# Optimization experiments

Measured on AMD Instinct MI355X. Metric: run time of the kernel, lower is better.

Reference implementation:

```python
import jax, jax.numpy as jnp
import numpy as np

N = 100000
E = 1600000
IN_FEATS = 128
N_HIDDEN = 128
N_CLASSES = 40
KLIST = [2, 2, 2]  # k=6 split over 3 layers as in DeepSGC.__init__


def setup_inputs() -> dict:
    key = jax.random.key(0)
    ks = jax.random.split(key, 10)
    features = jax.random.normal(ks[0], (N, IN_FEATS), dtype=jnp.float32)
    src = jax.random.randint(ks[1], (E,), 0, N, dtype=jnp.int64 if jax.config.jax_enable_x64 else jnp.int32)
    dst = jax.random.randint(ks[2], (E,), 0, N, dtype=jnp.int64 if jax.config.jax_enable_x64 else jnp.int32)
    def glorot(k, fan_in, fan_out):
        lim = (6.0 / (fan_in + fan_out)) ** 0.5
        return jax.random.uniform(k, (fan_in, fan_out), jnp.float32, -lim, lim)
    W1 = glorot(ks[3], IN_FEATS, N_HIDDEN)
    b1 = jnp.zeros((N_HIDDEN,), jnp.float32)
    W2 = glorot(ks[4], N_HIDDEN, N_HIDDEN)
    b2 = jnp.zeros((N_HIDDEN,), jnp.float32)
    W3 = glorot(ks[5], N_HIDDEN, N_CLASSES)
    b3 = jnp.zeros((N_CLASSES,), jnp.float32)
    return {"features": features, "src": src, "dst": dst,
            "W1": W1, "b1": b1, "W2": W2, "b2": b2, "W3": W3, "b3": b3}


def _propagate(h, src, dst, norm, k):
    # k hops of symmetric-normalized adjacency SpMM: h <- D^{-1/2} A D^{-1/2} h
    for _ in range(k):
        h = h * norm  # pre-scale [N, d]
        h = jax.ops.segment_sum(h[src], dst, num_segments=N)  # scatter-add over edges
        h = h * norm  # post-scale
    return h


def reference(features, src, dst, W1, b1, W2, b2, W3, b3):
    # in-degree based symmetric norm, clamped to >= 1 (as DGL SGConv)
    deg = jax.ops.segment_sum(jnp.ones((E,), jnp.float32), dst, num_segments=N)
    norm = jax.lax.rsqrt(jnp.clip(deg, 1.0))[:, None]  # [N, 1]

    h = features
    # layer 1: SGConv(k=2) + relu (dropout p=0 -> identity)
    h = _propagate(h, src, dst, norm, KLIST[0]) @ W1 + b1
    h = jax.nn.relu(h)
    # layer 2
    h = _propagate(h, src, dst, norm, KLIST[1]) @ W2 + b2
    h = jax.nn.relu(h)
    # layer 3 (no activation)
    h = _propagate(h, src, dst, norm, KLIST[2]) @ W3 + b3
    return h
```

## Files before the change

kernel.cpp:

```cpp
#include <hip/hip_runtime.h>
#include <hip/hip_bf16.h>


typedef __attribute__((ext_vector_type(8))) short short8v;
typedef __attribute__((ext_vector_type(4))) float f32x4;
typedef __attribute__((ext_vector_type(2))) unsigned int u32x2;

#define SBLK 128

__device__ __forceinline__ unsigned short f2bf(float x) {
    unsigned int u = __builtin_bit_cast(unsigned int, x);
    unsigned int r = u + 0x7fffu + ((u >> 16) & 1u);
    return (unsigned short)(r >> 16);
}
__device__ __forceinline__ float bf2f(unsigned short h) {
    unsigned int u = ((unsigned int)h) << 16;
    return __builtin_bit_cast(float, u);
}


__global__ void __launch_bounds__(256) deg_rank_kernel(const int* __restrict__ dst,
                                                       int* __restrict__ deg,
                                                       int* __restrict__ rank, int E) {
    int e = blockIdx.x * blockDim.x + threadIdx.x;
    if (e < E) rank[e] = atomicAdd(&deg[dst[e]], 1);
}

__global__ void __launch_bounds__(256) scanA_kernel(const int* __restrict__ deg,
                                                    int* __restrict__ rowptr,
                                                    int* __restrict__ bsum,
                                                    float* __restrict__ norm,
                                                    int n, int seg) {
    __shared__ int ws[4];
    __shared__ int carry;
    int b = blockIdx.x;
    int start = b * seg;
    int finish = start + seg; if (finish > n) finish = n;
    int t = threadIdx.x, lane = t & 63, w = t >> 6;
    if (t == 0) carry = 0;
    __syncthreads();
    for (int base = start; base < finish; base += 256) {
        int i = base + t;
        int v = 0;
        if (i < finish) {
            v = deg[i];
            norm[i] = rsqrtf((float)(v < 1 ? 1 : v));
        }
        int x = v;
        #pragma unroll
        for (int off = 1; off < 64; off <<= 1) {
            int y = __shfl_up(x, off, 64);
            if (lane >= off) x += y;
        }
        if (lane == 63) ws[w] = x;
        __syncthreads();
        int woff = 0;
        #pragma unroll
        for (int k = 0; k < 4; ++k) if (k < w) woff += ws[k];
        if (i < finish) rowptr[i] = carry + woff + x - v;
        int tot = ws[0] + ws[1] + ws[2] + ws[3];
        __syncthreads();
        if (t == 0) carry += tot;
        __syncthreads();
    }
    if (t == 0) bsum[b] = carry;
}

__global__ void __launch_bounds__(256) scanC_kernel(int* __restrict__ rowptr,
                                                    const int* __restrict__ bsum,
                                                    int n, int seg) {
    __shared__ int tmp[SBLK + 1];
    int b = blockIdx.x, t = threadIdx.x;
    if (t < SBLK) tmp[t] = bsum[t];
    __syncthreads();
    if (t == 0) {
        int s = 0;
        #pragma unroll 4
        for (int i = 0; i < SBLK; ++i) { int v = tmp[i]; tmp[i] = s; s += v; }
        tmp[SBLK] = s;
    }
    __syncthreads();
    int add = tmp[b];
    int start = b * seg;
    int finish = start + seg; if (finish > n) finish = n;
    for (int i = start + t; i < finish; i += 256) rowptr[i] += add;
    if (b == 0 && t == 0) rowptr[n] = tmp[SBLK];
}

__global__ void __launch_bounds__(256) fill_kernel(const int* __restrict__ src,
                                                   const int* __restrict__ dst,
                                                   const int* __restrict__ rowptr,
                                                   const int* __restrict__ rank,
                                                   int* __restrict__ col, int E) {
    int e = blockIdx.x * blockDim.x + threadIdx.x;
    if (e < E) col[rowptr[dst[e]] + rank[e]] = src[e];
}


__global__ void __launch_bounds__(256) xquant_kernel(const float4* __restrict__ x,
                                                     const float* __restrict__ norm,
                                                     u32x2* __restrict__ xq,
                                                     float* __restrict__ S,
                                                     float* __restrict__ Sn,
                                                     int n) {
    int gw = (blockIdx.x * blockDim.x + threadIdx.x) >> 6;
    int lane = threadIdx.x & 63, half = lane >> 5, l32 = lane & 31;
    int node = gw * 2 + half;
    if (node >= n) return;
    float4 v = x[(size_t)node * 32 + l32];
    float m = fmaxf(fmaxf(fabsf(v.x), fabsf(v.y)), fmaxf(fabsf(v.z), fabsf(v.w)));
    #pragma unroll
    for (int s = 1; s < 32; s <<= 1) m = fmaxf(m, __shfl_xor(m, s));
    float sraw = fmaxf(m, 1e-30f);
    float inv = 32767.f / sraw;
    float sv = sraw * (1.f / 32767.f);
    int a0 = (int)rintf(fminf(fmaxf(v.x * inv, -32767.f), 32767.f));
    int a1 = (int)rintf(fminf(fmaxf(v.y * inv, -32767.f), 32767.f));
    int a2 = (int)rintf(fminf(fmaxf(v.z * inv, -32767.f), 32767.f));
    int a3 = (int)rintf(fminf(fmaxf(v.w * inv, -32767.f), 32767.f));
    u32x2 p = {(unsigned)(a0 & 0xffff) | ((unsigned)a1 << 16),
               (unsigned)(a2 & 0xffff) | ((unsigned)a3 << 16)};
    __builtin_nontemporal_store(p, &xq[(size_t)node * 32 + l32]);
    if (l32 == 0) { S[node] = sv; Sn[node] = sv * norm[node]; }
}


template <int EPI>
__global__ void __launch_bounds__(256) spmm128_q(const u32x2* __restrict__ hq,
                                                 const float* __restrict__ esc,
                                                 const int* __restrict__ rp,
                                                 const int* __restrict__ col,
                                                 const float* __restrict__ norm,
                                                 u32x2* __restrict__ outq,
                                                 float* __restrict__ So,
                                                 float* __restrict__ Sno,
                                                 u32x2* __restrict__ Hi,
                                                 u32x2* __restrict__ Lo,
                                                 int n) {
    int wid = (blockIdx.x * blockDim.x + threadIdx.x) >> 6;
    if (wid >= n) return;
    int lane = threadIdx.x & 63, half = lane >> 5, l32 = lane & 31;
    int beg = rp[wid], end = rp[wid + 1];
    f32x4 acc = {0.f, 0.f, 0.f, 0.f};
    if (beg < end) {
        int last = end - 1;
        for (int e = beg; e < end; e += 8) {
            int i0 = e + half, i1 = e + 2 + half, i2 = e + 4 + half, i3 = e + 6 + half;
            int i0c = i0 < end ? i0 : last;
            int i1c = i1 < end ? i1 : last;
            int i2c = i2 < end ? i2 : last;
            int i3c = i3 < end ? i3 : last;
            int u0 = col[i0c], u1 = col[i1c], u2 = col[i2c], u3 = col[i3c];
            float s0 = i0 < end ? esc[u0] : 0.f;
            float s1 = i1 < end ? esc[u1] : 0.f;
            float s2 = i2 < end ? esc[u2] : 0.f;
            float s3 = i3 < end ? esc[u3] : 0.f;
            u32x2 q0 = hq[(size_t)u0 * 32 + l32];
            u32x2 q1 = hq[(size_t)u1 * 32 + l32];
            u32x2 q2 = hq[(size_t)u2 * 32 + l32];
            u32x2 q3 = hq[(size_t)u3 * 32 + l32];
            acc.x += (float)(short)(q0.x) * s0;
            acc.y += (float)((int)q0.x >> 16) * s0;
            acc.z += (float)(short)(q0.y) * s0;
            acc.w += (float)((int)q0.y >> 16) * s0;
            acc.x += (float)(short)(q1.x) * s1;
            acc.y += (float)((int)q1.x >> 16) * s1;
            acc.z += (float)(short)(q1.y) * s1;
            acc.w += (float)((int)q1.y >> 16) * s1;
            acc.x += (float)(short)(q2.x) * s2;
            acc.y += (float)((int)q2.x >> 16) * s2;
            acc.z += (float)(short)(q2.y) * s2;
            acc.w += (float)((int)q2.y >> 16) * s2;
            acc.x += (float)(short)(q3.x) * s3;
            acc.y += (float)((int)q3.x >> 16) * s3;
            acc.z += (float)(short)(q3.y) * s3;
            acc.w += (float)((int)q3.y >> 16) * s3;
        }
    }
    acc.x += __shfl_xor(acc.x, 32);
    acc.y += __shfl_xor(acc.y, 32);
    acc.z += __shfl_xor(acc.z, 32);
    acc.w += __shfl_xor(acc.w, 32);
    float nv = norm[wid];
    if (EPI == 0) {
        float f = nv * nv;
        acc.x *= f; acc.y *= f; acc.z *= f; acc.w *= f;
        float m = fmaxf(fmaxf(fabsf(acc.x), fabsf(acc.y)), fmaxf(fabsf(acc.z), fabsf(acc.w)));
        #pragma unroll
        for (int s = 1; s < 64; s <<= 1) m = fmaxf(m, __shfl_xor(m, s));
        float sraw = fmaxf(m, 1e-30f);
        float inv = 32767.f / sraw;
        float sv = sraw * (1.f / 32767.f);
        if (half == 0) {
            int a0 = (int)rintf(fminf(fmaxf(acc.x * inv, -32767.f), 32767.f));
            int a1 = (int)rintf(fminf(fmaxf(acc.y * inv, -32767.f), 32767.f));
            int a2 = (int)rintf(fminf(fmaxf(acc.z * inv, -32767.f), 32767.f));
            int a3 = (int)rintf(fminf(fmaxf(acc.w * inv, -32767.f), 32767.f));
            u32x2 p = {(unsigned)(a0 & 0xffff) | ((unsigned)a1 << 16),
                       (unsigned)(a2 & 0xffff) | ((unsigned)a3 << 16)};
            __builtin_nontemporal_store(p, &outq[(size_t)wid * 32 + l32]);
        }
        if (lane == 0) { So[wid] = sv; Sno[wid] = sv * nv; }
    } else {
        if (half == 0) {
            float v0 = acc.x * nv, v1 = acc.y * nv, v2 = acc.z * nv, v3 = acc.w * nv;
            unsigned short h0 = f2bf(v0), h1 = f2bf(v1), h2 = f2bf(v2), h3 = f2bf(v3);
            unsigned short l0 = f2bf(v0 - bf2f(h0)), l1 = f2bf(v1 - bf2f(h1));
            unsigned short l2 = f2bf(v2 - bf2f(h2)), l3 = f2bf(v3 - bf2f(h3));
            u32x2 hp = {(unsigned int)h0 | ((unsigned int)h1 << 16),
                        (unsigned int)h2 | ((unsigned int)h3 << 16)};
            u32x2 lp = {(unsigned int)l0 | ((unsigned int)l1 << 16),
                        (unsigned int)l2 | ((unsigned int)l3 << 16)};
            __builtin_nontemporal_store(hp, &Hi[(size_t)wid * 32 + l32]);
            __builtin_nontemporal_store(lp, &Lo[(size_t)wid * 32 + l32]);
        }
    }
}

template <int FIRST, int BIAS>
__global__ void __launch_bounds__(256) spmm40_kernel(const f32x4* __restrict__ hin,
                                                     f32x4* __restrict__ hout,
                                                     const int* __restrict__ rp,
                                                     const int* __restrict__ col,
                                                     const float* __restrict__ norm,
                                                     const float* __restrict__ b3,
                                                     int n) {
    int wid = (blockIdx.x * blockDim.x + threadIdx.x) >> 6;
    if (wid >= n) return;
    int lane = threadIdx.x & 63;
    int slot = lane / 10;
    int t = lane % 10;
    bool active = slot < 6;
    int beg = rp[wid], end = rp[wid + 1];
    f32x4 acc = {0.f, 0.f, 0.f, 0.f};
    if (beg < end) {
        int last = end - 1;
        for (int base = beg; base < end; base += 18) {
            int i0 = base + slot, i1 = base + 6 + slot, i2 = base + 12 + slot;
            int i0c = (active && i0 < end) ? i0 : last;
            int i1c = (active && i1 < end) ? i1 : last;
            int i2c = (active && i2 < end) ? i2 : last;
            int u0 = col[i0c], u1 = col[i1c], u2 = col[i2c];
            float s0 = (active && i0 < end) ? (FIRST ? norm[u0] : 1.f) : 0.f;
            float s1 = (active && i1 < end) ? (FIRST ? norm[u1] : 1.f) : 0.f;
            float s2 = (active && i2 < end) ? (FIRST ? norm[u2] : 1.f) : 0.f;
            f32x4 x0 = hin[(size_t)u0 * 10 + t];
            f32x4 x1 = hin[(size_t)u1 * 10 + t];
            f32x4 x2 = hin[(size_t)u2 * 10 + t];
            acc.x += x0.x * s0; acc.y += x0.y * s0; acc.z += x0.z * s0; acc.w += x0.w * s0;
            acc.x += x1.x * s1; acc.y += x1.y * s1; acc.z += x1.z * s1; acc.w += x1.w * s1;
            acc.x += x2.x * s2; acc.y += x2.y * s2; acc.z += x2.z * s2; acc.w += x2.w * s2;
        }
    }
    f32x4 tot = acc;
    #pragma unroll
    for (int k = 1; k < 6; ++k) {
        int srcl = (lane % 10) + ((slot + k) % 6) * 10;
        tot.x += __shfl(acc.x, srcl);
        tot.y += __shfl(acc.y, srcl);
        tot.z += __shfl(acc.z, srcl);
        tot.w += __shfl(acc.w, srcl);
    }
    if (slot == 0) {
        float nv = norm[wid];
        float f = FIRST ? nv * nv : nv;
        f32x4 o = {tot.x * f, tot.y * f, tot.z * f, tot.w * f};
        if (BIAS) {
            f32x4 bv = ((const f32x4*)b3)[t];
            o.x += bv.x; o.y += bv.y; o.z += bv.z; o.w += bv.w;
        }
        __builtin_nontemporal_store(o, &hout[(size_t)wid * 10 + t]);
    }
}


__device__ __forceinline__ void wprep_one(const float* __restrict__ W,
                                          short* __restrict__ Wh,
                                          short* __restrict__ Wl,
                                          int ncols, int CF, int i) {
    int j = i & 7;
    int lane = (i >> 3) & 63;
    int f = i >> 9;
    int cf = f % CF, ks = f / CF;
    int k = ks * 32 + 8 * (lane >> 4) + j;
    int c = cf * 16 + (lane & 15);
    float v = (c < ncols) ? W[k * ncols + c] : 0.f;
    unsigned short h = f2bf(v);
    unsigned short l = f2bf(v - bf2f(h));
    Wh[i] = (short)h;
    Wl[i] = (short)l;
}

__global__ void __launch_bounds__(256) wprep_all(const float* __restrict__ W1,
                                                 const float* __restrict__ W2,
                                                 const float* __restrict__ W3,
                                                 short* __restrict__ W1h, short* __restrict__ W1l,
                                                 short* __restrict__ W2h, short* __restrict__ W2l,
                                                 short* __restrict__ W3h, short* __restrict__ W3l) {
    int i = blockIdx.x * blockDim.x + threadIdx.x;
    if (i < 16384) wprep_one(W1, W1h, W1l, 128, 8, i);
    else if (i < 32768) wprep_one(W2, W2h, W2l, 128, 8, i - 16384);
    else if (i < 38912) wprep_one(W3, W3h, W3l, 40, 3, i - 32768);
}


template <int MODE>
__global__ void __launch_bounds__(256) gemm_mfma128(const unsigned short* __restrict__ Ahi,
                                                    const unsigned short* __restrict__ Alo,
                                                    const short8v* __restrict__ Wh,
                                                    const short8v* __restrict__ Wl,
                                                    const float* __restrict__ bias,
                                                    const float* __restrict__ norm,
                                                    unsigned short* __restrict__ Cq,
                                                    float* __restrict__ So,
                                                    float* __restrict__ Sno,
                                                    unsigned short* __restrict__ Chi,
                                                    unsigned short* __restrict__ Clo,
                                                    int n) {
    int lane = threadIdx.x & 63;
    int wid = threadIdx.x >> 6;
    int r0 = blockIdx.x * 64 + wid * 16;
    if (r0 >= n) return;
    int arow = r0 + (lane & 15);
    if (arow > n - 1) arow = n - 1;
    int kbase = 8 * (lane >> 4);
    f32x4 acc[8];
    #pragma unroll
    for (int i = 0; i < 8; ++i) acc[i] = (f32x4){0.f, 0.f, 0.f, 0.f};
    #pragma unroll
    for (int ks = 0; ks < 4; ++ks) {
        short8v ah = *(const short8v*)(Ahi + (size_t)arow * 128 + ks * 32 + kbase);
        short8v al = *(const short8v*)(Alo + (size_t)arow * 128 + ks * 32 + kbase);
        #pragma unroll
        for (int cf = 0; cf < 8; ++cf) {
            short8v bh = Wh[(ks * 8 + cf) * 64 + lane];
            short8v bl = Wl[(ks * 8 + cf) * 64 + lane];
            acc[cf] = __builtin_amdgcn_mfma_f32_16x16x32_bf16(ah, bh, acc[cf], 0, 0, 0);
            acc[cf] = __builtin_amdgcn_mfma_f32_16x16x32_bf16(al, bh, acc[cf], 0, 0, 0);
            acc[cf] = __builtin_amdgcn_mfma_f32_16x16x32_bf16(ah, bl, acc[cf], 0, 0, 0);
        }
    }
    int rbase = r0 + (lane >> 4) * 4;
    int c0 = lane & 15;
    float bc[8];
    #pragma unroll
    for (int cf = 0; cf < 8; ++cf) bc[cf] = bias[cf * 16 + c0];

    if (MODE == 0) {
        float mq[4] = {0.f, 0.f, 0.f, 0.f};
        #pragma unroll
        for (int cf = 0; cf < 8; ++cf) {
            #pragma unroll
            for (int q = 0; q < 4; ++q)
                mq[q] = fmaxf(mq[q], fmaxf(acc[cf][q] + bc[cf], 0.f));
        }
        #pragma unroll
        for (int s = 1; s < 16; s <<= 1) {
            #pragma unroll
            for (int q = 0; q < 4; ++q) mq[q] = fmaxf(mq[q], __shfl_xor(mq[q], s));
        }
        float invq[4], svq[4];
        #pragma unroll
        for (int q = 0; q < 4; ++q) {
            float sraw = fmaxf(mq[q], 1e-30f);
            invq[q] = 32767.f / sraw;
            svq[q] = sraw * (1.f / 32767.f);
        }
        #pragma unroll
        for (int cf = 0; cf < 8; ++cf) {
            int colc = cf * 16 + c0;
            #pragma unroll
            for (int q = 0; q < 4; ++q) {
                int row = rbase + q;
                if (row >= n) continue;
                float v = fmaxf(acc[cf][q] + bc[cf], 0.f);
                int qi = (int)rintf(fminf(v * invq[q], 32767.f));
                Cq[(size_t)row * 128 + colc] = (unsigned short)qi;
            }
        }
        if (c0 == 0) {
            #pragma unroll
            for (int q = 0; q < 4; ++q) {
                int row = rbase + q;
                if (row < n) { So[row] = svq[q]; Sno[row] = svq[q] * norm[row]; }
            }
        }
    } else {
        #pragma unroll
        for (int cf = 0; cf < 8; ++cf) {
            int colc = cf * 16 + c0;
            #pragma unroll
            for (int q = 0; q < 4; ++q) {
                int row = rbase + q;
                if (row >= n) continue;
                float v = fmaxf(acc[cf][q] + bc[cf], 0.f);
                unsigned short h = f2bf(v);
                unsigned short l = f2bf(v - bf2f(h));
                Chi[(size_t)row * 128 + colc] = h;
                Clo[(size_t)row * 128 + colc] = l;
            }
        }
    }
}

__global__ void __launch_bounds__(256) gemm_mfma40(const unsigned short* __restrict__ Ahi,
                                                   const unsigned short* __restrict__ Alo,
                                                   const short8v* __restrict__ Wh,
                                                   const short8v* __restrict__ Wl,
                                                   float* __restrict__ Cf, int n) {
    int lane = threadIdx.x & 63;
    int wid = threadIdx.x >> 6;
    int r0 = blockIdx.x * 64 + wid * 16;
    if (r0 >= n) return;
    int arow = r0 + (lane & 15);
    if (arow > n - 1) arow = n - 1;
    int kbase = 8 * (lane >> 4);
    f32x4 acc[3];
    #pragma unroll
    for (int i = 0; i < 3; ++i) acc[i] = (f32x4){0.f, 0.f, 0.f, 0.f};
    #pragma unroll
    for (int ks = 0; ks < 4; ++ks) {
        short8v ah = *(const short8v*)(Ahi + (size_t)arow * 128 + ks * 32 + kbase);
        short8v al = *(const short8v*)(Alo + (size_t)arow * 128 + ks * 32 + kbase);
        #pragma unroll
        for (int cf = 0; cf < 3; ++cf) {
            short8v bh = Wh[(ks * 3 + cf) * 64 + lane];
            short8v bl = Wl[(ks * 3 + cf) * 64 + lane];
            acc[cf] = __builtin_amdgcn_mfma_f32_16x16x32_bf16(ah, bh, acc[cf], 0, 0, 0);
            acc[cf] = __builtin_amdgcn_mfma_f32_16x16x32_bf16(al, bh, acc[cf], 0, 0, 0);
            acc[cf] = __builtin_amdgcn_mfma_f32_16x16x32_bf16(ah, bl, acc[cf], 0, 0, 0);
        }
    }
    int rbase = r0 + (lane >> 4) * 4;
    int c0 = lane & 15;
    #pragma unroll
    for (int cf = 0; cf < 3; ++cf) {
        int colc = cf * 16 + c0;
        if (colc >= 40) continue;
        #pragma unroll
        for (int q = 0; q < 4; ++q) {
            int row = rbase + q;
            if (row >= n) continue;
            Cf[(size_t)row * 40 + colc] = acc[cf][q];
        }
    }
}


extern "C" void kernel_launch(void* const* d_in, const int* in_sizes, int n_in,
                              void* d_out, int out_size, void* d_ws, size_t ws_size,
                              hipStream_t stream) {
    const float* features = (const float*)d_in[0];
    const int*   src      = (const int*)d_in[1];
    const int*   dst      = (const int*)d_in[2];
    const float* W1 = (const float*)d_in[3];
    const float* b1 = (const float*)d_in[4];
    const float* W2 = (const float*)d_in[5];
    const float* b2 = (const float*)d_in[6];
    const float* W3 = (const float*)d_in[7];
    const float* b3 = (const float*)d_in[8];
    float* out = (float*)d_out;

    const int N = in_sizes[0] / 128;
    const int E = in_sizes[1];

    char* ws = (char*)d_ws;
    size_t off = 0;
    auto alloc = [&](size_t bytes) -> void* {
        void* p = ws + off;
        off += (bytes + 511) & ~(size_t)511;
        return p;
    };
    u32x2* Xq  = (u32x2*)alloc((size_t)N * 32 * sizeof(u32x2));
    u32x2* F1q = (u32x2*)alloc((size_t)N * 32 * sizeof(u32x2));
    u32x2* F2q = (u32x2*)alloc((size_t)N * 32 * sizeof(u32x2));
    unsigned short* Hi = (unsigned short*)alloc((size_t)N * 128 * sizeof(unsigned short));
    unsigned short* Lo = (unsigned short*)alloc((size_t)N * 128 * sizeof(unsigned short));
    float* Sx  = (float*)alloc((size_t)N * sizeof(float));
    float* Snx = (float*)alloc((size_t)N * sizeof(float));
    float* S1  = (float*)alloc((size_t)N * sizeof(float));
    float* Sn1 = (float*)alloc((size_t)N * sizeof(float));
    float* S2  = (float*)alloc((size_t)N * sizeof(float));
    float* Sn2 = (float*)alloc((size_t)N * sizeof(float));
    int*   col    = (int*)alloc((size_t)E * sizeof(int));
    int*   deg    = (int*)alloc((size_t)N * sizeof(int));
    int*   rowptr = (int*)alloc((size_t)(N + 1) * sizeof(int));
    float* norm   = (float*)alloc((size_t)N * sizeof(float));
    int*   bsum   = (int*)alloc((size_t)(SBLK + 2) * sizeof(int));
    short* W1h = (short*)alloc(16384 * sizeof(short));
    short* W1l = (short*)alloc(16384 * sizeof(short));
    short* W2h = (short*)alloc(16384 * sizeof(short));
    short* W2l = (short*)alloc(16384 * sizeof(short));
    short* W3h = (short*)alloc(6144 * sizeof(short));
    short* W3l = (short*)alloc(6144 * sizeof(short));
    int*   rank = (int*)Hi;
    float* G40a = (float*)F2q;
    float* G40b = (float*)Xq;

    const int seg = (N + SBLK - 1) / SBLK;
    const int eblocks = (E + 255) / 256;

    hipMemsetAsync(deg, 0, (size_t)N * sizeof(int), stream);
    deg_rank_kernel<<<eblocks, 256, 0, stream>>>(dst, deg, rank, E);
    scanA_kernel<<<SBLK, 256, 0, stream>>>(deg, rowptr, bsum, norm, N, seg);
    scanC_kernel<<<SBLK, 256, 0, stream>>>(rowptr, bsum, N, seg);
    fill_kernel<<<eblocks, 256, 0, stream>>>(src, dst, rowptr, rank, col, E);

    wprep_all<<<(38912 + 255) / 256, 256, 0, stream>>>(W1, W2, W3, W1h, W1l, W2h, W2l, W3h, W3l);
    {
        int waves2 = (N + 1) / 2;
        int xblocks = (waves2 * 64 + 255) / 256;
        xquant_kernel<<<xblocks, 256, 0, stream>>>((const float4*)features, norm, Xq, Sx, Snx, N);
    }

    const int spmm_blocks = (N * 64 + 255) / 256;
    const int gemm_blocks = (N + 63) / 64;

    spmm128_q<0><<<spmm_blocks, 256, 0, stream>>>(Xq, Snx, rowptr, col, norm,
                                                  F1q, S1, Sn1, nullptr, nullptr, N);
    spmm128_q<1><<<spmm_blocks, 256, 0, stream>>>(F1q, S1, rowptr, col, norm,
                                                  nullptr, nullptr, nullptr, (u32x2*)Hi, (u32x2*)Lo, N);
    gemm_mfma128<0><<<gemm_blocks, 256, 0, stream>>>(Hi, Lo, (const short8v*)W1h, (const short8v*)W1l,
                                                     b1, norm, (unsigned short*)F2q, S2, Sn2,
                                                     nullptr, nullptr, N);

    spmm128_q<0><<<spmm_blocks, 256, 0, stream>>>(F2q, Sn2, rowptr, col, norm,
                                                  F1q, S1, Sn1, nullptr, nullptr, N);
    spmm128_q<1><<<spmm_blocks, 256, 0, stream>>>(F1q, S1, rowptr, col, norm,
                                                  nullptr, nullptr, nullptr, (u32x2*)Hi, (u32x2*)Lo, N);
    gemm_mfma128<1><<<gemm_blocks, 256, 0, stream>>>(Hi, Lo, (const short8v*)W2h, (const short8v*)W2l,
                                                     b2, norm, nullptr, nullptr, nullptr,
                                                     Hi, Lo, N);

    gemm_mfma40<<<gemm_blocks, 256, 0, stream>>>(Hi, Lo, (const short8v*)W3h, (const short8v*)W3l, G40a, N);
    spmm40_kernel<1, 0><<<spmm_blocks, 256, 0, stream>>>((const f32x4*)G40a, (f32x4*)G40b, rowptr, col, norm, nullptr, N);
    spmm40_kernel<0, 1><<<spmm_blocks, 256, 0, stream>>>((const f32x4*)G40b, (f32x4*)out, rowptr, col, norm, b3, N);
}
```

Baseline: 639.6 us.

## Quantize layer-3 path to int16 with per-row scales and deepen SpMM gather unroll

Layer 2's GEMM now writes int16-quantized rows with per-row scales instead of bf16 hi/lo pairs. The 40-wide GEMM dequantizes these on the fly, and the two final 40-column SpMMs gather int16 rows instead of fp32. This halves the bytes moved in the last layer's gathers and GEMM input. The 128-wide SpMM gather loop is also unrolled from 4 to 8 edges per half-wave to keep more loads in flight. The cost is extra quantization error in the last layer and higher register pressure in the SpMM.

After: 690.6 us. 1.08x slower.

```diff
diff --git a/kernel.cpp b/kernel.cpp
--- a/kernel.cpp
+++ b/kernel.cpp
@@ -100,7 +100,6 @@
 __global__ void __launch_bounds__(256) xquant_kernel(const float4* __restrict__ x,
                                                      const float* __restrict__ norm,
                                                      u32x2* __restrict__ xq,
-                                                     float* __restrict__ S,
                                                      float* __restrict__ Sn,
                                                      int n) {
     int gw = (blockIdx.x * blockDim.x + threadIdx.x) >> 6;
@@ -121,7 +120,7 @@
     u32x2 p = {(unsigned)(a0 & 0xffff) | ((unsigned)a1 << 16),
                (unsigned)(a2 & 0xffff) | ((unsigned)a3 << 16)};
     __builtin_nontemporal_store(p, &xq[(size_t)node * 32 + l32]);
-    if (l32 == 0) { S[node] = sv; Sn[node] = sv * norm[node]; }
+    if (l32 == 0) Sn[node] = sv * norm[node];
 }
 
 
@@ -133,7 +132,6 @@
                                                  const float* __restrict__ norm,
                                                  u32x2* __restrict__ outq,
                                                  float* __restrict__ So,
-                                                 float* __restrict__ Sno,
                                                  u32x2* __restrict__ Hi,
                                                  u32x2* __restrict__ Lo,
                                                  int n) {
@@ -144,37 +142,24 @@
     f32x4 acc = {0.f, 0.f, 0.f, 0.f};
     if (beg < end) {
         int last = end - 1;
-        for (int e = beg; e < end; e += 8) {
-            int i0 = e + half, i1 = e + 2 + half, i2 = e + 4 + half, i3 = e + 6 + half;
-            int i0c = i0 < end ? i0 : last;
-            int i1c = i1 < end ? i1 : last;
-            int i2c = i2 < end ? i2 : last;
-            int i3c = i3 < end ? i3 : last;
-            int u0 = col[i0c], u1 = col[i1c], u2 = col[i2c], u3 = col[i3c];
-            float s0 = i0 < end ? esc[u0] : 0.f;
-            float s1 = i1 < end ? esc[u1] : 0.f;
-            float s2 = i2 < end ? esc[u2] : 0.f;
-            float s3 = i3 < end ? esc[u3] : 0.f;
-            u32x2 q0 = hq[(size_t)u0 * 32 + l32];
-            u32x2 q1 = hq[(size_t)u1 * 32 + l32];
-            u32x2 q2 = hq[(size_t)u2 * 32 + l32];
-            u32x2 q3 = hq[(size_t)u3 * 32 + l32];
-            acc.x += (float)(short)(q0.x) * s0;
-            acc.y += (float)((int)q0.x >> 16) * s0;
-            acc.z += (float)(short)(q0.y) * s0;
-            acc.w += (float)((int)q0.y >> 16) * s0;
-            acc.x += (float)(short)(q1.x) * s1;
-            acc.y += (float)((int)q1.x >> 16) * s1;
-            acc.z += (float)(short)(q1.y) * s1;
-            acc.w += (float)((int)q1.y >> 16) * s1;
-            acc.x += (float)(short)(q2.x) * s2;
-            acc.y += (float)((int)q2.x >> 16) * s2;
-            acc.z += (float)(short)(q2.y) * s2;
-            acc.w += (float)((int)q2.y >> 16) * s2;
-            acc.x += (float)(short)(q3.x) * s3;
-            acc.y += (float)((int)q3.x >> 16) * s3;
-            acc.z += (float)(short)(q3.y) * s3;
-            acc.w += (float)((int)q3.y >> 16) * s3;
+        for (int e = beg; e < end; e += 16) {
+            float s[8];
+            u32x2 q[8];
+            #pragma unroll
+            for (int k = 0; k < 8; ++k) {
+                int i = e + 2 * k + half;
+                int ic = i < end ? i : last;
+                int u = col[ic];
+                s[k] = i < end ? esc[u] : 0.f;
+                q[k] = hq[(size_t)u * 32 + l32];
+            }
+            #pragma unroll
+            for (int k = 0; k < 8; ++k) {
+                acc.x += (float)(short)(q[k].x) * s[k];
+                acc.y += (float)((int)q[k].x >> 16) * s[k];
+                acc.z += (float)(short)(q[k].y) * s[k];
+                acc.w += (float)((int)q[k].y >> 16) * s[k];
+            }
         }
     }
     acc.x += __shfl_xor(acc.x, 32);
@@ -200,7 +185,7 @@
                        (unsigned)(a2 & 0xffff) | ((unsigned)a3 << 16)};
             __builtin_nontemporal_store(p, &outq[(size_t)wid * 32 + l32]);
         }
-        if (lane == 0) { So[wid] = sv; Sno[wid] = sv * nv; }
+        if (lane == 0) So[wid] = sv;
     } else {
         if (half == 0) {
             float v0 = acc.x * nv, v1 = acc.y * nv, v2 = acc.z * nv, v3 = acc.w * nv;
@@ -217,14 +202,18 @@
     }
 }
 
-template <int FIRST, int BIAS>
-__global__ void __launch_bounds__(256) spmm40_kernel(const f32x4* __restrict__ hin,
-                                                     f32x4* __restrict__ hout,
-                                                     const int* __restrict__ rp,
-                                                     const int* __restrict__ col,
-                                                     const float* __restrict__ norm,
-                                                     const float* __restrict__ b3,
-                                                     int n) {
+
+template <int EPI>
+__global__ void __launch_bounds__(256) spmm40_q(const u32x2* __restrict__ hq,
+                                                const float* __restrict__ esc,
+                                                const int* __restrict__ rp,
+                                                const int* __restrict__ col,
+                                                const float* __restrict__ norm,
+                                                u32x2* __restrict__ outq,
+                                                float* __restrict__ So,
+                                                f32x4* __restrict__ outf,
+                                                const float* __restrict__ b3,
+                                                int n) {
     int wid = (blockIdx.x * blockDim.x + threadIdx.x) >> 6;
     if (wid >= n) return;
     int lane = threadIdx.x & 63;
@@ -236,40 +225,63 @@
     if (beg < end) {
         int last = end - 1;
         for (int base = beg; base < end; base += 18) {
-            int i0 = base + slot, i1 = base + 6 + slot, i2 = base + 12 + slot;
-            int i0c = (active && i0 < end) ? i0 : last;
-            int i1c = (active && i1 < end) ? i1 : last;
-            int i2c = (active && i2 < end) ? i2 : last;
-            int u0 = col[i0c], u1 = col[i1c], u2 = col[i2c];
-            float s0 = (active && i0 < end) ? (FIRST ? norm[u0] : 1.f) : 0.f;
-            float s1 = (active && i1 < end) ? (FIRST ? norm[u1] : 1.f) : 0.f;
-            float s2 = (active && i2 < end) ? (FIRST ? norm[u2] : 1.f) : 0.f;
-            f32x4 x0 = hin[(size_t)u0 * 10 + t];
-            f32x4 x1 = hin[(size_t)u1 * 10 + t];
-            f32x4 x2 = hin[(size_t)u2 * 10 + t];
-            acc.x += x0.x * s0; acc.y += x0.y * s0; acc.z += x0.z * s0; acc.w += x0.w * s0;
-            acc.x += x1.x * s1; acc.y += x1.y * s1; acc.z += x1.z * s1; acc.w += x1.w * s1;
-            acc.x += x2.x * s2; acc.y += x2.y * s2; acc.z += x2.z * s2; acc.w += x2.w * s2;
+            float s[3];
+            u32x2 q[3];
+            #pragma unroll
+            for (int k = 0; k < 3; ++k) {
+                int i = base + 6 * k + slot;
+                int ic = (active && i < end) ? i : last;
+                int u = col[ic];
+                s[k] = (active && i < end) ? esc[u] : 0.f;
+                q[k] = hq[(size_t)u * 10 + t];
+            }
+            #pragma unroll
+            for (int k = 0; k < 3; ++k) {
+                acc.x += (float)(short)(q[k].x) * s[k];
+                acc.y += (float)((int)q[k].x >> 16) * s[k];
+                acc.z += (float)(short)(q[k].y) * s[k];
+                acc.w += (float)((int)q[k].y >> 16) * s[k];
+            }
         }
     }
     f32x4 tot = acc;
     #pragma unroll
     for (int k = 1; k < 6; ++k) {
-        int srcl = (lane % 10) + ((slot + k) % 6) * 10;
+        int srcl = t + ((slot + k) % 6) * 10;
         tot.x += __shfl(acc.x, srcl);
         tot.y += __shfl(acc.y, srcl);
         tot.z += __shfl(acc.z, srcl);
         tot.w += __shfl(acc.w, srcl);
     }
-    if (slot == 0) {
-        float nv = norm[wid];
-        float f = FIRST ? nv * nv : nv;
-        f32x4 o = {tot.x * f, tot.y * f, tot.z * f, tot.w * f};
-        if (BIAS) {
+    float nv = norm[wid];
+    if (EPI == 0) {
+        float f = nv * nv;
+        f32x4 v = {tot.x * f, tot.y * f, tot.z * f, tot.w * f};
+        float m = (slot < 6)
+                ? fmaxf(fmaxf(fabsf(v.x), fabsf(v.y)), fmaxf(fabsf(v.z), fabsf(v.w)))
+                : 0.f;
+        #pragma unroll
+        for (int s = 1; s < 64; s <<= 1) m = fmaxf(m, __shfl_xor(m, s));
+        float sraw = fmaxf(m, 1e-30f);
+        float inv = 32767.f / sraw;
+        float sv = sraw * (1.f / 32767.f);
+        if (slot == 0) {
+            int a0 = (int)rintf(fminf(fmaxf(v.x * inv, -32767.f), 32767.f));
+            int a1 = (int)rintf(fminf(fmaxf(v.y * inv, -32767.f), 32767.f));
+            int a2 = (int)rintf(fminf(fmaxf(v.z * inv, -32767.f), 32767.f));
+            int a3 = (int)rintf(fminf(fmaxf(v.w * inv, -32767.f), 32767.f));
+            u32x2 p = {(unsigned)(a0 & 0xffff) | ((unsigned)a1 << 16),
+                       (unsigned)(a2 & 0xffff) | ((unsigned)a3 << 16)};
+            __builtin_nontemporal_store(p, &outq[(size_t)wid * 10 + t]);
+        }
+        if (lane == 0) So[wid] = sv;
+    } else {
+        if (slot == 0) {
             f32x4 bv = ((const f32x4*)b3)[t];
-            o.x += bv.x; o.y += bv.y; o.z += bv.z; o.w += bv.w;
-        }
-        __builtin_nontemporal_store(o, &hout[(size_t)wid * 10 + t]);
+            f32x4 o = {tot.x * nv + bv.x, tot.y * nv + bv.y,
+                       tot.z * nv + bv.z, tot.w * nv + bv.w};
+            __builtin_nontemporal_store(o, &outf[(size_t)wid * 10 + t]);
+        }
     }
 }
 
@@ -304,7 +316,6 @@
 }
 
 
-template <int MODE>
 __global__ void __launch_bounds__(256) gemm_mfma128(const unsigned short* __restrict__ Ahi,
                                                     const unsigned short* __restrict__ Alo,
                                                     const short8v* __restrict__ Wh,
@@ -314,8 +325,6 @@
                                                     unsigned short* __restrict__ Cq,
                                                     float* __restrict__ So,
                                                     float* __restrict__ Sno,
-                                                    unsigned short* __restrict__ Chi,
-                                                    unsigned short* __restrict__ Clo,
                                                     int n) {
     int lane = threadIdx.x & 63;
     int wid = threadIdx.x >> 6;
@@ -346,68 +355,55 @@
     #pragma unroll
     for (int cf = 0; cf < 8; ++cf) bc[cf] = bias[cf * 16 + c0];
 
-    if (MODE == 0) {
-        float mq[4] = {0.f, 0.f, 0.f, 0.f};
-        #pragma unroll
-        for (int cf = 0; cf < 8; ++cf) {
-            #pragma unroll
-            for (int q = 0; q < 4; ++q)
-                mq[q] = fmaxf(mq[q], fmaxf(acc[cf][q] + bc[cf], 0.f));
-        }
-        #pragma unroll
-        for (int s = 1; s < 16; s <<= 1) {
-            #pragma unroll
-            for (int q = 0; q < 4; ++q) mq[q] = fmaxf(mq[q], __shfl_xor(mq[q], s));
-        }
-        float invq[4], svq[4];
+    float mq[4] = {0.f, 0.f, 0.f, 0.f};
+    #pragma unroll
+    for (int cf = 0; cf < 8; ++cf) {
+        #pragma unroll
+        for (int q = 0; q < 4; ++q)
+            mq[q] = fmaxf(mq[q], fmaxf(acc[cf][q] + bc[cf], 0.f));
+    }
+    #pragma unroll
+    for (int s = 1; s < 16; s <<= 1) {
+        #pragma unroll
+        for (int q = 0; q < 4; ++q) mq[q] = fmaxf(mq[q], __shfl_xor(mq[q], s));
+    }
+    float invq[4], svq[4];
+    #pragma unroll
+    for (int q = 0; q < 4; ++q) {
+        float sraw = fmaxf(mq[q], 1e-30f);
+        invq[q] = 32767.f / sraw;
+        svq[q] = sraw * (1.f / 32767.f);
+    }
+    #pragma unroll
+    for (int cf = 0; cf < 8; ++cf) {
+        int colc = cf * 16 + c0;
         #pragma unroll
         for (int q = 0; q < 4; ++q) {
-            float sraw = fmaxf(mq[q], 1e-30f);
-            invq[q] = 32767.f / sraw;
-            svq[q] = sraw * (1.f / 32767.f);
-        }
-        #pragma unroll
-        for (int cf = 0; cf < 8; ++cf) {
-            int colc = cf * 16 + c0;
-            #pragma unroll
-            for (int q = 0; q < 4; ++q) {
-                int row = rbase + q;
-                if (row >= n) continue;
-                float v = fmaxf(acc[cf][q] + bc[cf], 0.f);
-                int qi = (int)rintf(fminf(v * invq[q], 32767.f));
-                Cq[(size_t)row * 128 + colc] = (unsigned short)qi;
-            }
-        }
-        if (c0 == 0) {
-            #pragma unroll
-            for (int q = 0; q < 4; ++q) {
-                int row = rbase + q;
-                if (row < n) { So[row] = svq[q]; Sno[row] = svq[q] * norm[row]; }
-            }
-        }
-    } else {
-        #pragma unroll
-        for (int cf = 0; cf < 8; ++cf) {
-            int colc = cf * 16 + c0;
-            #pragma unroll
-            for (int q = 0; q < 4; ++q) {
-                int row = rbase + q;
-                if (row >= n) continue;
-                float v = fmaxf(acc[cf][q] + bc[cf], 0.f);
-                unsigned short h = f2bf(v);
-                unsigned short l = f2bf(v - bf2f(h));
-                Chi[(size_t)row * 128 + colc] = h;
-                Clo[(size_t)row * 128 + colc] = l;
-            }
-        }
-    }
-}
-
-__global__ void __launch_bounds__(256) gemm_mfma40(const unsigned short* __restrict__ Ahi,
-                                                   const unsigned short* __restrict__ Alo,
+            int row = rbase + q;
+            if (row >= n) continue;
+            float v = fmaxf(acc[cf][q] + bc[cf], 0.f);
+            int qi = (int)rintf(fminf(v * invq[q], 32767.f));
+            Cq[(size_t)row * 128 + colc] = (unsigned short)qi;
+        }
+    }
+    if (c0 == 0) {
+        #pragma unroll
+        for (int q = 0; q < 4; ++q) {
+            int row = rbase + q;
+            if (row < n) { So[row] = svq[q]; Sno[row] = svq[q] * norm[row]; }
+        }
+    }
+}
+
+__global__ void __launch_bounds__(256) gemm_mfma40(const unsigned short* __restrict__ Aq,
+                                                   const float* __restrict__ SA,
                                                    const short8v* __restrict__ Wh,
                                                    const short8v* __restrict__ Wl,
-                                                   float* __restrict__ Cf, int n) {
+                                                   const float* __restrict__ norm,
+                                                   unsigned short* __restrict__ Cq,
+                                                   float* __restrict__ S3,
+                                                   float* __restrict__ Sn3,
+                                                   int n) {
     int lane = threadIdx.x & 63;
     int wid = threadIdx.x >> 6;
     int r0 = blockIdx.x * 64 + wid * 16;
@@ -415,13 +411,23 @@
     int arow = r0 + (lane & 15);
     if (arow > n - 1) arow = n - 1;
     int kbase = 8 * (lane >> 4);
+    float sA = SA[arow];
     f32x4 acc[3];
     #pragma unroll
     for (int i = 0; i < 3; ++i) acc[i] = (f32x4){0.f, 0.f, 0.f, 0.f};
     #pragma unroll
     for (int ks = 0; ks < 4; ++ks) {
-        short8v ah = *(const short8v*)(Ahi + (size_t)arow * 128 + ks * 32 + kbase);
-        short8v al = *(const short8v*)(Alo + (size_t)arow * 128 + ks * 32 + kbase);
+        short8v qv = *(const short8v*)(Aq + (size_t)arow * 128 + ks * 32 + kbase);
+        short8v ah, al;
+        #pragma unroll
+        for (int j = 0; j < 8; ++j) {
+            float v = (float)qv[j] * sA;
+            unsigned int uv = __builtin_bit_cast(unsigned int, v);
+            unsigned short hi = (unsigned short)(uv >> 16);
+            float r = v - bf2f(hi);
+            ah[j] = (short)hi;
+            al[j] = (short)f2bf(r);
+        }
         #pragma unroll
         for (int cf = 0; cf < 3; ++cf) {
             short8v bh = Wh[(ks * 3 + cf) * 64 + lane];
@@ -433,6 +439,27 @@
     }
     int rbase = r0 + (lane >> 4) * 4;
     int c0 = lane & 15;
+    float mq[4] = {0.f, 0.f, 0.f, 0.f};
+    #pragma unroll
+    for (int cf = 0; cf < 3; ++cf) {
+        int colc = cf * 16 + c0;
+        if (colc < 40) {
+            #pragma unroll
+            for (int q = 0; q < 4; ++q) mq[q] = fmaxf(mq[q], fabsf(acc[cf][q]));
+        }
+    }
+    #pragma unroll
+    for (int s = 1; s < 16; s <<= 1) {
+        #pragma unroll
+        for (int q = 0; q < 4; ++q) mq[q] = fmaxf(mq[q], __shfl_xor(mq[q], s));
+    }
+    float invq[4], svq[4];
+    #pragma unroll
+    for (int q = 0; q < 4; ++q) {
+        float sraw = fmaxf(mq[q], 1e-30f);
+        invq[q] = 32767.f / sraw;
+        svq[q] = sraw * (1.f / 32767.f);
+    }
     #pragma unroll
     for (int cf = 0; cf < 3; ++cf) {
         int colc = cf * 16 + c0;
@@ -441,7 +468,16 @@
         for (int q = 0; q < 4; ++q) {
             int row = rbase + q;
             if (row >= n) continue;
-            Cf[(size_t)row * 40 + colc] = acc[cf][q];
+            float v = acc[cf][q];
+            int qi = (int)rintf(fminf(fmaxf(v * invq[q], -32767.f), 32767.f));
+            Cq[(size_t)row * 40 + colc] = (unsigned short)qi;
+        }
+    }
+    if (c0 == 0) {
+        #pragma unroll
+        for (int q = 0; q < 4; ++q) {
+            int row = rbase + q;
+            if (row < n) { S3[row] = svq[q]; Sn3[row] = svq[q] * norm[row]; }
         }
     }
 }
@@ -471,17 +507,17 @@
         off += (bytes + 511) & ~(size_t)511;
         return p;
     };
-    u32x2* Xq  = (u32x2*)alloc((size_t)N * 32 * sizeof(u32x2));
-    u32x2* F1q = (u32x2*)alloc((size_t)N * 32 * sizeof(u32x2));
-    u32x2* F2q = (u32x2*)alloc((size_t)N * 32 * sizeof(u32x2));
+    u32x2* QA = (u32x2*)alloc((size_t)N * 32 * sizeof(u32x2));
+    u32x2* QB = (u32x2*)alloc((size_t)N * 32 * sizeof(u32x2));
     unsigned short* Hi = (unsigned short*)alloc((size_t)N * 128 * sizeof(unsigned short));
     unsigned short* Lo = (unsigned short*)alloc((size_t)N * 128 * sizeof(unsigned short));
-    float* Sx  = (float*)alloc((size_t)N * sizeof(float));
     float* Snx = (float*)alloc((size_t)N * sizeof(float));
-    float* S1  = (float*)alloc((size_t)N * sizeof(float));
-    float* Sn1 = (float*)alloc((size_t)N * sizeof(float));
-    float* S2  = (float*)alloc((size_t)N * sizeof(float));
-    float* Sn2 = (float*)alloc((size_t)N * sizeof(float));
+    float* Sk  = (float*)alloc((size_t)N * sizeof(float));
+    float* Sg  = (float*)alloc((size_t)N * sizeof(float));
+    float* Sng = (float*)alloc((size_t)N * sizeof(float));
+    float* S3  = (float*)alloc((size_t)N * sizeof(float));
+    float* Sn3 = (float*)alloc((size_t)N * sizeof(float));
+    float* S4  = (float*)alloc((size_t)N * sizeof(float));
     int*   col    = (int*)alloc((size_t)E * sizeof(int));
     int*   deg    = (int*)alloc((size_t)N * sizeof(int));
     int*   rowptr = (int*)alloc((size_t)(N + 1) * sizeof(int));
@@ -494,8 +530,8 @@
     short* W3h = (short*)alloc(6144 * sizeof(short));
     short* W3l = (short*)alloc(6144 * sizeof(short));
     int*   rank = (int*)Hi;
-    float* G40a = (float*)F2q;
-    float* G40b = (float*)Xq;
+    u32x2* G1 = (u32x2*)QB;
+    u32x2* G2 = (u32x2*)Hi;
 
     const int seg = (N + SBLK - 1) / SBLK;
     const int eblocks = (E + 255) / 256;
@@ -510,29 +546,31 @@
     {
         int waves2 = (N + 1) / 2;
         int xblocks = (waves2 * 64 + 255) / 256;
-        xquant_kernel<<<xblocks, 256, 0, stream>>>((const float4*)features, norm, Xq, Sx, Snx, N);
+        xquant_kernel<<<xblocks, 256, 0, stream>>>((const float4*)features, norm, QA, Snx, N);
     }
 
     const int spmm_blocks = (N * 64 + 255) / 256;
     const int gemm_blocks = (N + 63) / 64;
 
-    spmm128_q<0><<<spmm_blocks, 256, 0, stream>>>(Xq, Snx, rowptr, col, norm,
-                                                  F1q, S1, Sn1, nullptr, nullptr, N);
-    spmm128_q<1><<<spmm_blocks, 256, 0, stream>>>(F1q, S1, rowptr, col, norm,
-                                                  nullptr, nullptr, nullptr, (u32x2*)Hi, (u32x2*)Lo, N);
-    gemm_mfma128<0><<<gemm_blocks, 256, 0, stream>>>(Hi, Lo, (const short8v*)W1h, (const short8v*)W1l,
-                                                     b1, norm, (unsigned short*)F2q, S2, Sn2,
-                                                     nullptr, nullptr, N);
-
-    spmm128_q<0><<<spmm_blocks, 256, 0, stream>>>(F2q, Sn2, rowptr, col, norm,
-                                                  F1q, S1, Sn1, nullptr, nullptr, N);
-    spmm128_q<1><<<spmm_blocks, 256, 0, stream>>>(F1q, S1, rowptr, col, norm,
-                                                  nullptr, nullptr, nullptr, (u32x2*)Hi, (u32x2*)Lo, N);
-    gemm_mfma128<1><<<gemm_blocks, 256, 0, stream>>>(Hi, Lo, (const short8v*)W2h, (const short8v*)W2l,
-                                                     b2, norm, nullptr, nullptr, nullptr,
-                                                     Hi, Lo, N);
-
-    gemm_mfma40<<<gemm_blocks, 256, 0, stream>>>(Hi, Lo, (const short8v*)W3h, (const short8v*)W3l, G40a, N);
-    spmm40_kernel<1, 0><<<spmm_blocks, 256, 0, stream>>>((const f32x4*)G40a, (f32x4*)G40b, rowptr, col, norm, nullptr, N);
-    spmm40_kernel<0, 1><<<spmm_blocks, 256, 0, stream>>>((const f32x4*)G40b, (f32x4*)out, rowptr, col, norm, b3, N);
-}
+    spmm128_q<0><<<spmm_blocks, 256, 0, stream>>>(QA, Snx, rowptr, col, norm,
+                                                  QB, Sk, nullptr, nullptr, N);
+    spmm128_q<1><<<spmm_blocks, 256, 0, stream>>>(QB, Sk, rowptr, col, norm,
+                                                  nullptr, nullptr, (u32x2*)Hi, (u32x2*)Lo, N);
+    gemm_mfma128<<<gemm_blocks, 256, 0, stream>>>(Hi, Lo, (const short8v*)W1h, (const short8v*)W1l,
+                                                  b1, norm, (unsigned short*)QA, Sg, Sng, N);
+
+    spmm128_q<0><<<spmm_blocks, 256, 0, stream>>>(QA, Sng, rowptr, col, norm,
+                                                  QB, Sk, nullptr, nullptr, N);
+    spmm128_q<1><<<spmm_blocks, 256, 0, stream>>>(QB, Sk, rowptr, col, norm,
+                                                  nullptr, nullptr, (u32x2*)Hi, (u32x2*)Lo, N);
+    gemm_mfma128<<<gemm_blocks, 256, 0, stream>>>(Hi, Lo, (const short8v*)W2h, (const short8v*)W2l,
+                                                  b2, norm, (unsigned short*)QA, Sg, Sng, N);
+
+    gemm_mfma40<<<gemm_blocks, 256, 0, stream>>>((const unsigned short*)QA, Sg,
+                                                 (const short8v*)W3h, (const short8v*)W3l,
+                                                 norm, (unsigned short*)G1, S3, Sn3, N);
+    spmm40_q<0><<<spmm_blocks, 256, 0, stream>>>(G1, Sn3, rowptr, col, norm,
+                                                 G2, S4, nullptr, nullptr, N);
+    spmm40_q<1><<<spmm_blocks, 256, 0, stream>>>(G2, S4, rowptr, col, norm,
+                                                 nullptr, nullptr, (f32x4*)out, b3, N);
+}
```
